# Kernel optimization log

Measured on AMD Instinct MI355X. Metric: run time of the kernel, lower is better.

Reference implementation:

```python
import jax, jax.numpy as jnp
import numpy as np

B, D, K = 65536, 512, 64
H1, H2 = 256, 128
START_TEMP, MIN_TEMP, NR_EPOCHS = 10.0, 0.1, 1000


def setup_inputs() -> dict:
    key = jax.random.key(0)
    ks = jax.random.split(key, 12)
    x = jax.random.normal(ks[0], (B, D), dtype=jnp.float32)
    label = jax.random.normal(ks[1], (B, 1), dtype=jnp.float32)
    u = jax.random.uniform(ks[2], (B, K), dtype=jnp.float32, minval=1e-6, maxval=1.0)
    # MLP params: D -> H1 -> H2 -> K (relu on hidden layers, bias everywhere)
    W1 = jax.random.normal(ks[3], (D, H1), dtype=jnp.float32) / np.sqrt(D)
    b1 = jnp.zeros((H1,), dtype=jnp.float32)
    W2 = jax.random.normal(ks[4], (H1, H2), dtype=jnp.float32) / np.sqrt(H1)
    b2 = jnp.zeros((H2,), dtype=jnp.float32)
    W3 = jax.random.normal(ks[5], (H2, K), dtype=jnp.float32) / np.sqrt(H2)
    b3 = jnp.zeros((K,), dtype=jnp.float32)
    # thetas ~ Uniform(0,1) per torch init.uniform_
    thetas = jax.random.uniform(ks[6], (D, K), dtype=jnp.float32)
    return {"x": x, "label": label, "u": u, "W1": W1, "b1": b1,
            "W2": W2, "b2": b2, "W3": W3, "b3": b3,
            "thetas": thetas, "epoch": 100}


def _current_temp(epoch):
    # exponential schedule: max(min_temp, start*(min/start)**(epoch/nr_epochs))
    t = START_TEMP * (MIN_TEMP / START_TEMP) ** (epoch / NR_EPOCHS)
    return jnp.maximum(jnp.float32(MIN_TEMP), jnp.float32(t))


def reference(x, label, u, W1, b1, W2, b2, W3, b3, thetas, epoch):
    # MLP -> logits [B, K]
    h = jax.nn.relu(x @ W1 + b1)
    h = jax.nn.relu(h @ W2 + b2)
    logits = h @ W3 + b3
    # Concrete (Gumbel-softmax) feature selection over the K candidate predictors
    xt = x @ thetas                      # [B, K]
    gumbel = -jnp.log(-jnp.log(u))
    temp = _current_temp(jnp.float32(epoch))
    weights = jax.nn.softmax((logits + gumbel) / temp, axis=1)
    # diagonal(xt @ weights.T) == row-wise dot product (O(B*K), not O(B^2*K))
    selected = jnp.sum(xt * weights, axis=1, keepdims=True)  # [B, 1]
    loss = jnp.mean((selected - label) ** 2)
    return loss
```

## Files before the change

kernel.cpp:

```cpp
#include <hip/hip_runtime.h>
#include <math.h>

#define Bn  65536
#define Dn  512
#define Kn  64
#define H1n 256
#define H2n 128
#define BM  16

typedef short bf16x8 __attribute__((ext_vector_type(8)));
typedef float floatx4 __attribute__((ext_vector_type(4)));

__device__ __forceinline__ unsigned short f2bf(float f) {
    unsigned u = __builtin_bit_cast(unsigned, f);
    u += 0x7FFF + ((u >> 16) & 1);
    return (unsigned short)(u >> 16);
}

__global__ __launch_bounds__(256)
void prep_k(const float* __restrict__ W1, const float* __restrict__ W2,
            const float* __restrict__ W3, const float* __restrict__ Th,
            unsigned short* __restrict__ ws)
{
    const int gid = blockIdx.x * 256 + threadIdx.x;
    if (gid < 131072) {
        const int s = gid, k = s >> 8, n = s & 255;
        const int dst = (((n >> 4) * 16 + (k >> 5)) * 64 + ((k >> 3) & 3) * 16 + (n & 15)) * 8 + (k & 7);
        ws[dst] = f2bf(W1[s]);
    } else if (gid < 163840) {
        const int s = gid - 131072, k = s >> 6, n = s & 63;
        const int dst = 131072 + (((n >> 4) * 16 + (k >> 5)) * 64 + ((k >> 3) & 3) * 16 + (n & 15)) * 8 + (k & 7);
        ws[dst] = f2bf(Th[s]);
    } else if (gid < 196608) {
        const int s = gid - 163840, k = s >> 7, n = s & 127;
        const int dst = 163840 + (((n >> 4) * 8 + (k >> 5)) * 64 + ((k >> 3) & 3) * 16 + (n & 15)) * 8 + (k & 7);
        ws[dst] = f2bf(W2[s]);
    } else if (gid < 204800) {
        const int s = gid - 196608, k = s >> 6, n = s & 63;
        const int dst = 196608 + (((n >> 4) * 4 + (k >> 5)) * 64 + ((k >> 3) & 3) * 16 + (n & 15)) * 8 + (k & 7);
        ws[dst] = f2bf(W3[s]);
    }
}

__global__ __launch_bounds__(1024)
void reduce_k(const float* __restrict__ p, float* __restrict__ out)
{
    __shared__ float sred[16];
    const int tid = threadIdx.x;
    float s = 0.f;
    #pragma unroll
    for (int i = 0; i < 16; ++i) s += p[tid + i * 1024];
    #pragma unroll
    for (int off = 32; off > 0; off >>= 1) s += __shfl_xor(s, off);
    if ((tid & 63) == 0) sred[tid >> 6] = s;
    __syncthreads();
    if (tid < 64) {
        float v = (tid < 16) ? sred[tid] : 0.f;
        #pragma unroll
        for (int off = 8; off > 0; off >>= 1) v += __shfl_xor(v, off);
        if (tid == 0) out[0] = v * (1.0f / (float)Bn);
    }
}

__global__ __launch_bounds__(256, 4)
void llp_mfma(const float* __restrict__ x,
              const float* __restrict__ label,
              const float* __restrict__ u,
              const float* __restrict__ b1, const float* __restrict__ b2,
              const float* __restrict__ b3,
              const unsigned short* __restrict__ W1f,
              const unsigned short* __restrict__ Tf,
              const unsigned short* __restrict__ W2f,
              const unsigned short* __restrict__ W3f,
              const int* __restrict__ epoch_p,
              float* __restrict__ partials)
{
    __shared__ char smem[28672];

    const int tid  = threadIdx.x;
    const int row0 = blockIdx.x * BM;
    const int w    = tid >> 6;
    const int lane = tid & 63;
    const int lrow = lane & 15;
    const int quad = lane >> 4;

    float upf[4], labpf[4];
    #pragma unroll
    for (int rr = 0; rr < 4; ++rr) {
        upf[rr]   = u[(size_t)(row0 + w * 4 + rr) * Kn + lane];
        labpf[rr] = label[row0 + w * 4 + rr];
    }

    {
        const float4* xg4 = (const float4*)(x + (size_t)row0 * Dn);
        #pragma unroll
        for (int i = 0; i < 8; ++i) {
            const int f = tid + i * 256;
            const float4 v = xg4[f];
            const int row = f >> 7, c4 = f & 127;
            const int kb = c4 >> 1, half = c4 & 1;
            ushort4 o;
            o.x = f2bf(v.x); o.y = f2bf(v.y); o.z = f2bf(v.z); o.w = f2bf(v.w);
            *(ushort4*)(smem + ((row * 64 + (kb ^ (row & 7))) << 4) + (half << 3)) = o;
        }
    }
    __syncthreads();

    const int ct0 = w * 4;
    floatx4 acc[4], xtac;
    #pragma unroll
    for (int t = 0; t < 4; ++t) {
        const float bv = b1[(ct0 + t) * 16 + lrow];
        acc[t] = (floatx4){bv, bv, bv, bv};
    }
    xtac = (floatx4){0.f, 0.f, 0.f, 0.f};

    #pragma unroll 4
    for (int ks = 0; ks < 16; ++ks) {
        const bf16x8 a = *(const bf16x8*)(smem +
                            ((lrow * 64 + ((ks * 4 + quad) ^ (lrow & 7))) << 4));
        #pragma unroll
        for (int t = 0; t < 4; ++t) {
            const bf16x8 b = *(const bf16x8*)(W1f + ((((ct0 + t) * 16 + ks) * 64 + lane) << 3));
            acc[t] = __builtin_amdgcn_mfma_f32_16x16x32_bf16(a, b, acc[t], 0, 0, 0);
        }
        const bf16x8 bt = *(const bf16x8*)(Tf + (((w * 16 + ks) * 64 + lane) << 3));
        xtac = __builtin_amdgcn_mfma_f32_16x16x32_bf16(a, bt, xtac, 0, 0, 0);
    }

    #pragma unroll
    for (int t = 0; t < 4; ++t) {
        const int col = (ct0 + t) * 16 + lrow;
        #pragma unroll
        for (int g = 0; g < 4; ++g) {
            const int orow = quad * 4 + g;
            *(unsigned short*)(smem + 16384 +
                ((orow * 32 + ((col >> 3) ^ (orow & 7))) << 4) + ((col & 7) << 1))
                = f2bf(fmaxf(acc[t][g], 0.0f));
        }
    }
    __syncthreads();

    {
        float* xtf = (float*)smem;
        #pragma unroll
        for (int g = 0; g < 4; ++g)
            xtf[(quad * 4 + g) * 68 + w * 16 + lrow] = xtac[g];
    }

    const int c2 = w * 2;
    floatx4 acc2[2];
    #pragma unroll
    for (int i = 0; i < 2; ++i) {
        const float bv = b2[(c2 + i) * 16 + lrow];
        acc2[i] = (floatx4){bv, bv, bv, bv};
    }
    #pragma unroll
    for (int ks = 0; ks < 8; ++ks) {
        const bf16x8 a = *(const bf16x8*)(smem + 16384 +
                            ((lrow * 32 + ((ks * 4 + quad) ^ (lrow & 7))) << 4));
        #pragma unroll
        for (int i = 0; i < 2; ++i) {
            const bf16x8 b = *(const bf16x8*)(W2f + ((((c2 + i) * 8 + ks) * 64 + lane) << 3));
            acc2[i] = __builtin_amdgcn_mfma_f32_16x16x32_bf16(a, b, acc2[i], 0, 0, 0);
        }
    }
    #pragma unroll
    for (int i = 0; i < 2; ++i) {
        const int col = (c2 + i) * 16 + lrow;
        #pragma unroll
        for (int g = 0; g < 4; ++g) {
            const int orow = quad * 4 + g;
            *(unsigned short*)(smem + 24576 +
                ((orow * 16 + ((col >> 3) ^ (orow & 7))) << 4) + ((col & 7) << 1))
                = f2bf(fmaxf(acc2[i][g], 0.0f));
        }
    }
    __syncthreads();

    floatx4 acc3;
    {
        const float bv = b3[w * 16 + lrow];
        acc3 = (floatx4){bv, bv, bv, bv};
    }
    #pragma unroll
    for (int ks = 0; ks < 4; ++ks) {
        const bf16x8 a = *(const bf16x8*)(smem + 24576 +
                            ((lrow * 16 + ((ks * 4 + quad) ^ (lrow & 7))) << 4));
        const bf16x8 b = *(const bf16x8*)(W3f + (((w * 4 + ks) * 64 + lane) << 3));
        acc3 = __builtin_amdgcn_mfma_f32_16x16x32_bf16(a, b, acc3, 0, 0, 0);
    }
    {
        float* lgf = (float*)(smem + 8192);
        #pragma unroll
        for (int g = 0; g < 4; ++g)
            lgf[(quad * 4 + g) * 68 + w * 16 + lrow] = acc3[g];
    }
    __syncthreads();

    {
        const float* xtf = (const float*)smem;
        const float* lgf = (const float*)(smem + 8192);
        const int ep = *epoch_p;
        const float tmp = 10.0f * powf(0.01f, (float)ep * 0.001f);
        const float inv_temp = 1.0f / fmaxf(0.1f, tmp);

        float partial = 0.0f;
        #pragma unroll
        for (int rr = 0; rr < 4; ++rr) {
            const int rw = w * 4 + rr;
            const float g = -logf(-logf(upf[rr]));
            float s = (lgf[rw * 68 + lane] + g) * inv_temp;
            float m = s;
            #pragma unroll
            for (int off = 32; off > 0; off >>= 1)
                m = fmaxf(m, __shfl_xor(m, off));
            const float e = expf(s - m);
            float sum = e;
            #pragma unroll
            for (int off = 32; off > 0; off >>= 1)
                sum += __shfl_xor(sum, off);
            float v = (e / sum) * xtf[rw * 68 + lane];
            #pragma unroll
            for (int off = 32; off > 0; off >>= 1)
                v += __shfl_xor(v, off);
            const float diff = v - labpf[rr];
            partial = fmaf(diff, diff, partial);
        }
        if (lane == 0)
            partials[blockIdx.x * 4 + w] = partial;
    }
}

extern "C" void kernel_launch(void* const* d_in, const int* in_sizes, int n_in,
                              void* d_out, int out_size, void* d_ws, size_t ws_size,
                              hipStream_t stream) {
    const float* x      = (const float*)d_in[0];
    const float* label  = (const float*)d_in[1];
    const float* u      = (const float*)d_in[2];
    const float* W1     = (const float*)d_in[3];
    const float* b1     = (const float*)d_in[4];
    const float* W2     = (const float*)d_in[5];
    const float* b2     = (const float*)d_in[6];
    const float* W3     = (const float*)d_in[7];
    const float* b3     = (const float*)d_in[8];
    const float* thetas = (const float*)d_in[9];
    const int*   epoch  = (const int*)d_in[10];
    float* out = (float*)d_out;

    unsigned short* wsb = (unsigned short*)d_ws;
    float* partials = (float*)(wsb + 204800);

    prep_k<<<800, 256, 0, stream>>>(W1, W2, W3, thetas, wsb);
    llp_mfma<<<Bn / BM, 256, 0, stream>>>(x, label, u, b1, b2, b3,
                                          wsb, wsb + 131072, wsb + 163840, wsb + 196608,
                                          epoch, partials);
    reduce_k<<<1, 1024, 0, stream>>>(partials, out);
}
```

Measured before the change: 308.9 us.

## Double row tile to 32 and software-pipeline MFMA operand loads

Each block now processes 32 rows instead of 16, so every weight fragment loaded from global memory feeds two MFMAs (one per 16-row tile), halving weight traffic per row. The K-loops of layers 1 and 2 are double-buffered: the next step's A/B fragments are loaded while the current MFMAs run. Shared memory grows to 48KB and launch bounds drop to 3 blocks per SM, and the number of partials and the reduction trip count are halved to match. The costs are higher register pressure and lower occupancy.

```diff
diff --git a/kernel.cpp b/kernel.cpp
--- a/kernel.cpp
+++ b/kernel.cpp
@@ -6,7 +6,7 @@
 #define Kn  64
 #define H1n 256
 #define H2n 128
-#define BM  16
+#define BM  32
 
 typedef short bf16x8 __attribute__((ext_vector_type(8)));
 typedef float floatx4 __attribute__((ext_vector_type(4)));
@@ -49,7 +49,7 @@
     const int tid = threadIdx.x;
     float s = 0.f;
     #pragma unroll
-    for (int i = 0; i < 16; ++i) s += p[tid + i * 1024];
+    for (int i = 0; i < 8; ++i) s += p[tid + i * 1024];
     #pragma unroll
     for (int off = 32; off > 0; off >>= 1) s += __shfl_xor(s, off);
     if ((tid & 63) == 0) sred[tid >> 6] = s;
@@ -62,7 +62,7 @@
     }
 }
 
-__global__ __launch_bounds__(256, 4)
+__global__ __launch_bounds__(256, 3)
 void llp_mfma(const float* __restrict__ x,
               const float* __restrict__ label,
               const float* __restrict__ u,
@@ -75,7 +75,7 @@
               const int* __restrict__ epoch_p,
               float* __restrict__ partials)
 {
-    __shared__ char smem[28672];
+    __shared__ char smem[49152];
 
     const int tid  = threadIdx.x;
     const int row0 = blockIdx.x * BM;
@@ -84,17 +84,17 @@
     const int lrow = lane & 15;
     const int quad = lane >> 4;
 
-    float upf[4], labpf[4];
-    #pragma unroll
-    for (int rr = 0; rr < 4; ++rr) {
-        upf[rr]   = u[(size_t)(row0 + w * 4 + rr) * Kn + lane];
-        labpf[rr] = label[row0 + w * 4 + rr];
+    float upf[8], labpf[8];
+    #pragma unroll
+    for (int rr = 0; rr < 8; ++rr) {
+        upf[rr]   = u[(size_t)(row0 + w * 8 + rr) * Kn + lane];
+        labpf[rr] = label[row0 + w * 8 + rr];
     }
 
     {
         const float4* xg4 = (const float4*)(x + (size_t)row0 * Dn);
         #pragma unroll
-        for (int i = 0; i < 8; ++i) {
+        for (int i = 0; i < 16; ++i) {
             const int f = tid + i * 256;
             const float4 v = xg4[f];
             const int row = f >> 7, c4 = f & 127;
@@ -107,36 +107,59 @@
     __syncthreads();
 
     const int ct0 = w * 4;
-    floatx4 acc[4], xtac;
+    floatx4 acc[2][5];
     #pragma unroll
     for (int t = 0; t < 4; ++t) {
         const float bv = b1[(ct0 + t) * 16 + lrow];
-        acc[t] = (floatx4){bv, bv, bv, bv};
-    }
-    xtac = (floatx4){0.f, 0.f, 0.f, 0.f};
-
-    #pragma unroll 4
+        acc[0][t] = (floatx4){bv, bv, bv, bv};
+        acc[1][t] = (floatx4){bv, bv, bv, bv};
+    }
+    acc[0][4] = (floatx4){0.f, 0.f, 0.f, 0.f};
+    acc[1][4] = (floatx4){0.f, 0.f, 0.f, 0.f};
+
+    bf16x8 aB[2][2], bB[2][5];
+    #pragma unroll
+    for (int rt = 0; rt < 2; ++rt)
+        aB[0][rt] = *(const bf16x8*)(smem +
+                        (((rt * 16 + lrow) * 64 + (quad ^ (lrow & 7))) << 4));
+    #pragma unroll
+    for (int t = 0; t < 4; ++t)
+        bB[0][t] = *(const bf16x8*)(W1f + ((((ct0 + t) * 16 + 0) * 64 + lane) << 3));
+    bB[0][4] = *(const bf16x8*)(Tf + (((w * 16 + 0) * 64 + lane) << 3));
+
+    #pragma unroll
     for (int ks = 0; ks < 16; ++ks) {
-        const bf16x8 a = *(const bf16x8*)(smem +
-                            ((lrow * 64 + ((ks * 4 + quad) ^ (lrow & 7))) << 4));
+        const int cur = ks & 1, nxt = cur ^ 1;
+        if (ks < 15) {
+            const int kn = ks + 1;
+            #pragma unroll
+            for (int rt = 0; rt < 2; ++rt)
+                aB[nxt][rt] = *(const bf16x8*)(smem +
+                    (((rt * 16 + lrow) * 64 + ((kn * 4 + quad) ^ (lrow & 7))) << 4));
+            #pragma unroll
+            for (int t = 0; t < 4; ++t)
+                bB[nxt][t] = *(const bf16x8*)(W1f + ((((ct0 + t) * 16 + kn) * 64 + lane) << 3));
+            bB[nxt][4] = *(const bf16x8*)(Tf + (((w * 16 + kn) * 64 + lane) << 3));
+        }
+        #pragma unroll
+        for (int t = 0; t < 5; ++t) {
+            acc[0][t] = __builtin_amdgcn_mfma_f32_16x16x32_bf16(aB[cur][0], bB[cur][t], acc[0][t], 0, 0, 0);
+            acc[1][t] = __builtin_amdgcn_mfma_f32_16x16x32_bf16(aB[cur][1], bB[cur][t], acc[1][t], 0, 0, 0);
+        }
+    }
+
+    #pragma unroll
+    for (int rt = 0; rt < 2; ++rt) {
         #pragma unroll
         for (int t = 0; t < 4; ++t) {
-            const bf16x8 b = *(const bf16x8*)(W1f + ((((ct0 + t) * 16 + ks) * 64 + lane) << 3));
-            acc[t] = __builtin_amdgcn_mfma_f32_16x16x32_bf16(a, b, acc[t], 0, 0, 0);
-        }
-        const bf16x8 bt = *(const bf16x8*)(Tf + (((w * 16 + ks) * 64 + lane) << 3));
-        xtac = __builtin_amdgcn_mfma_f32_16x16x32_bf16(a, bt, xtac, 0, 0, 0);
-    }
-
-    #pragma unroll
-    for (int t = 0; t < 4; ++t) {
-        const int col = (ct0 + t) * 16 + lrow;
-        #pragma unroll
-        for (int g = 0; g < 4; ++g) {
-            const int orow = quad * 4 + g;
-            *(unsigned short*)(smem + 16384 +
-                ((orow * 32 + ((col >> 3) ^ (orow & 7))) << 4) + ((col & 7) << 1))
-                = f2bf(fmaxf(acc[t][g], 0.0f));
+            const int col = (ct0 + t) * 16 + lrow;
+            #pragma unroll
+            for (int g = 0; g < 4; ++g) {
+                const int orow = rt * 16 + quad * 4 + g;
+                *(unsigned short*)(smem + 32768 +
+                    ((orow * 32 + ((col >> 3) ^ (orow & 7))) << 4) + ((col & 7) << 1))
+                    = f2bf(fmaxf(acc[rt][t][g], 0.0f));
+            }
         }
     }
     __syncthreads();
@@ -144,71 +167,101 @@
     {
         float* xtf = (float*)smem;
         #pragma unroll
-        for (int g = 0; g < 4; ++g)
-            xtf[(quad * 4 + g) * 68 + w * 16 + lrow] = xtac[g];
-    }
-
-    const int c2 = w * 2;
-    floatx4 acc2[2];
+        for (int rt = 0; rt < 2; ++rt)
+            #pragma unroll
+            for (int g = 0; g < 4; ++g)
+                xtf[(rt * 16 + quad * 4 + g) * 68 + w * 16 + lrow] = acc[rt][4][g];
+    }
+
+    const int c20 = w * 2;
+    floatx4 acc2[2][2];
     #pragma unroll
     for (int i = 0; i < 2; ++i) {
-        const float bv = b2[(c2 + i) * 16 + lrow];
-        acc2[i] = (floatx4){bv, bv, bv, bv};
-    }
+        const float bv = b2[(c20 + i) * 16 + lrow];
+        acc2[0][i] = (floatx4){bv, bv, bv, bv};
+        acc2[1][i] = (floatx4){bv, bv, bv, bv};
+    }
+    bf16x8 a2[2][2], b2B[2][2];
+    #pragma unroll
+    for (int rt = 0; rt < 2; ++rt)
+        a2[0][rt] = *(const bf16x8*)(smem + 32768 +
+                        (((rt * 16 + lrow) * 32 + (quad ^ (lrow & 7))) << 4));
+    #pragma unroll
+    for (int i = 0; i < 2; ++i)
+        b2B[0][i] = *(const bf16x8*)(W2f + ((((c20 + i) * 8 + 0) * 64 + lane) << 3));
+
     #pragma unroll
     for (int ks = 0; ks < 8; ++ks) {
-        const bf16x8 a = *(const bf16x8*)(smem + 16384 +
-                            ((lrow * 32 + ((ks * 4 + quad) ^ (lrow & 7))) << 4));
+        const int cur = ks & 1, nxt = cur ^ 1;
+        if (ks < 7) {
+            const int kn = ks + 1;
+            #pragma unroll
+            for (int rt = 0; rt < 2; ++rt)
+                a2[nxt][rt] = *(const bf16x8*)(smem + 32768 +
+                    (((rt * 16 + lrow) * 32 + ((kn * 4 + quad) ^ (lrow & 7))) << 4));
+            #pragma unroll
+            for (int i = 0; i < 2; ++i)
+                b2B[nxt][i] = *(const bf16x8*)(W2f + ((((c20 + i) * 8 + kn) * 64 + lane) << 3));
+        }
         #pragma unroll
         for (int i = 0; i < 2; ++i) {
-            const bf16x8 b = *(const bf16x8*)(W2f + ((((c2 + i) * 8 + ks) * 64 + lane) << 3));
-            acc2[i] = __builtin_amdgcn_mfma_f32_16x16x32_bf16(a, b, acc2[i], 0, 0, 0);
-        }
-    }
-    #pragma unroll
-    for (int i = 0; i < 2; ++i) {
-        const int col = (c2 + i) * 16 + lrow;
-        #pragma unroll
-        for (int g = 0; g < 4; ++g) {
-            const int orow = quad * 4 + g;
-            *(unsigned short*)(smem + 24576 +
-                ((orow * 16 + ((col >> 3) ^ (orow & 7))) << 4) + ((col & 7) << 1))
-                = f2bf(fmaxf(acc2[i][g], 0.0f));
-        }
-    }
-    __syncthreads();
-
-    floatx4 acc3;
+            acc2[0][i] = __builtin_amdgcn_mfma_f32_16x16x32_bf16(a2[cur][0], b2B[cur][i], acc2[0][i], 0, 0, 0);
+            acc2[1][i] = __builtin_amdgcn_mfma_f32_16x16x32_bf16(a2[cur][1], b2B[cur][i], acc2[1][i], 0, 0, 0);
+        }
+    }
+    #pragma unroll
+    for (int rt = 0; rt < 2; ++rt) {
+        #pragma unroll
+        for (int i = 0; i < 2; ++i) {
+            const int col = (c20 + i) * 16 + lrow;
+            #pragma unroll
+            for (int g = 0; g < 4; ++g) {
+                const int orow = rt * 16 + quad * 4 + g;
+                *(unsigned short*)(smem + 17408 +
+                    ((orow * 16 + ((col >> 3) ^ (orow & 7))) << 4) + ((col & 7) << 1))
+                    = f2bf(fmaxf(acc2[rt][i][g], 0.0f));
+            }
+        }
+    }
+    __syncthreads();
+
+    floatx4 acc3[2];
     {
         const float bv = b3[w * 16 + lrow];
-        acc3 = (floatx4){bv, bv, bv, bv};
+        acc3[0] = (floatx4){bv, bv, bv, bv};
+        acc3[1] = (floatx4){bv, bv, bv, bv};
     }
     #pragma unroll
     for (int ks = 0; ks < 4; ++ks) {
-        const bf16x8 a = *(const bf16x8*)(smem + 24576 +
-                            ((lrow * 16 + ((ks * 4 + quad) ^ (lrow & 7))) << 4));
-        const bf16x8 b = *(const bf16x8*)(W3f + (((w * 4 + ks) * 64 + lane) << 3));
-        acc3 = __builtin_amdgcn_mfma_f32_16x16x32_bf16(a, b, acc3, 0, 0, 0);
-    }
-    {
-        float* lgf = (float*)(smem + 8192);
-        #pragma unroll
-        for (int g = 0; g < 4; ++g)
-            lgf[(quad * 4 + g) * 68 + w * 16 + lrow] = acc3[g];
+        const bf16x8 bb = *(const bf16x8*)(W3f + (((w * 4 + ks) * 64 + lane) << 3));
+        #pragma unroll
+        for (int rt = 0; rt < 2; ++rt) {
+            const bf16x8 aa = *(const bf16x8*)(smem + 17408 +
+                (((rt * 16 + lrow) * 16 + ((ks * 4 + quad) ^ (lrow & 7))) << 4));
+            acc3[rt] = __builtin_amdgcn_mfma_f32_16x16x32_bf16(aa, bb, acc3[rt], 0, 0, 0);
+        }
+    }
+    {
+        float* lgf = (float*)(smem + 8704);
+        #pragma unroll
+        for (int rt = 0; rt < 2; ++rt)
+            #pragma unroll
+            for (int g = 0; g < 4; ++g)
+                lgf[(rt * 16 + quad * 4 + g) * 68 + w * 16 + lrow] = acc3[rt][g];
     }
     __syncthreads();
 
     {
         const float* xtf = (const float*)smem;
-        const float* lgf = (const float*)(smem + 8192);
+        const float* lgf = (const float*)(smem + 8704);
         const int ep = *epoch_p;
         const float tmp = 10.0f * powf(0.01f, (float)ep * 0.001f);
         const float inv_temp = 1.0f / fmaxf(0.1f, tmp);
 
         float partial = 0.0f;
         #pragma unroll
-        for (int rr = 0; rr < 4; ++rr) {
-            const int rw = w * 4 + rr;
+        for (int rr = 0; rr < 8; ++rr) {
+            const int rw = w * 8 + rr;
             const float g = -logf(-logf(upf[rr]));
             float s = (lgf[rw * 68 + lane] + g) * inv_temp;
             float m = s;
```

After: 269.6 us. -12.7%, faster.
